# Performance work log

Measured on AMD Instinct MI355X. Metric: run time of the kernel, lower is better.

Reference implementation:

```python
import jax, jax.numpy as jnp
from jax import lax
import numpy as np

ALPHA = 4.0  # spikingjelly surrogate.Sigmoid default alpha
TAU = 2.0
VTH = 1.0

@jax.custom_vjp
def heaviside(x):
    return (x >= 0).astype(x.dtype)

def _h_fwd(x):
    return heaviside(x), x

def _h_bwd(x, g):
    s = jax.nn.sigmoid(ALPHA * x)
    return (g * ALPHA * s * (1.0 - s),)

heaviside.defvjp(_h_fwd, _h_bwd)

def lif(x_seq):
    # MultiStepLIFNode: v += (x - v)/tau, hard reset to 0, detach_reset=True
    def step(v, x):
        v = v + (x - v) / TAU
        s = heaviside(v - VTH)
        v = v * (1.0 - lax.stop_gradient(s))
        return v, s
    _, spikes = lax.scan(step, jnp.zeros_like(x_seq[0]), x_seq)
    return spikes

def ss2d(x, in_w, conv_w, x_proj_w, dt_w, dt_b, A_logs, Ds, ln_g, ln_b, out_w):
    Bn, D, H, W = x.shape
    L = H * W
    x = jnp.einsum('bchw,dc->bdhw', x, in_w)                 # in_proj 1x1, no bias
    x = lax.conv_general_dilated(x, conv_w, (1, 1), 'SAME',
                                 feature_group_count=D)      # depthwise 3x3, no bias
    x = jax.nn.silu(x)
    x0 = x.reshape(Bn, D, L)
    x1 = x.transpose(0, 1, 3, 2).reshape(Bn, D, L)           # W-major scan
    xs = jnp.stack([x0, x1, x0[..., ::-1], x1[..., ::-1]], axis=1)  # (B,4,D,L) cross-scan
    R = dt_w.shape[-1]
    dbl = jnp.einsum('bkdl,krd->bkrl', xs, x_proj_w)         # (B,4,R+2N,L), N=1
    dts, Bs, Cs = dbl[:, :, :R], dbl[:, :, R:R + 1], dbl[:, :, R + 1:R + 2]
    dt = jnp.einsum('bkrl,kdr->bkdl', dts, dt_w)
    dt = jax.nn.softplus(dt + dt_b[None, :, :, None])
    A = -jnp.exp(A_logs)                                     # (4,D), d_state=1
    da = jnp.exp(dt * A[None, :, :, None])
    db = dt * Bs * xs                                        # Bs broadcasts over D
    def comb(l, r):
        al, bl = l
        ar, br = r
        return al * ar, bl * ar + br
    _, h = lax.associative_scan(comb, (da, db), axis=-1)     # h_t = da_t*h_{t-1} + db_t
    ys = Cs * h + Ds[None, :, :, None] * xs                  # (B,4,D,L)
    ya = ys[:, 0] + ys[:, 2, :, ::-1]
    yb = (ys[:, 1] + ys[:, 3, :, ::-1]).reshape(Bn, D, W, H).transpose(0, 1, 3, 2)
    y = ya.reshape(Bn, D, H, W) + yb                         # cross-merge
    mu = y.mean(axis=1, keepdims=True)                       # LayerNorm over channels
    var = jnp.mean((y - mu) ** 2, axis=1, keepdims=True)
    y = (y - mu) * lax.rsqrt(var + 1e-5) * ln_g[None, :, None, None] + ln_b[None, :, None, None]
    return jnp.einsum('bdhw,cd->bchw', y, out_w)             # out_proj 1x1, no bias

def spike_mamba(x, in_proj_w, in_proj_b, conv_w, conv_b, ssm_in_w, ssm_conv_w,
                x_proj_w, dt_proj_w, dt_proj_b, A_logs, Ds, ln_g, ln_b, out_proj_w):
    T, B, C, H, W = x.shape
    TB = T * B
    L = H * W
    xf = x.reshape(TB, C, L).transpose(0, 2, 1)              # (TB, L, C)
    xp = (xf @ in_proj_w.T + in_proj_b).transpose(0, 2, 1).reshape(TB, C, H, W)
    xsnn = lif(xp)                                           # LIF scans over dim 0 (= T*B, as in source)
    xc = lax.conv_general_dilated(xsnn, conv_w, (1, 1), 'SAME') + conv_b[None, :, None, None]
    xc = jax.nn.silu(xc)
    y = ss2d(xc, ssm_in_w, ssm_conv_w, x_proj_w, dt_proj_w, dt_proj_b,
             A_logs, Ds, ln_g, ln_b, out_proj_w)
    y = lif(y.reshape(T, B, C, H, W))                        # LIF over T
    return y * x

def setup_inputs() -> dict:
    key = jax.random.key(0)
    ks = jax.random.split(key, 10)
    T, B, C, H, W = 4, 4, 96, 56, 56
    R, K = 6, 4  # dt_rank=ceil(C/16), 4 scan directions
    s = 1.0 / np.sqrt(C)
    return {
        'x': jax.random.normal(ks[0], (T, B, C, H, W), jnp.float32),
        'in_proj_w': jax.random.normal(ks[1], (C, C), jnp.float32) * s,
        'in_proj_b': jnp.zeros((C,), jnp.float32),
        'conv_w': jax.random.normal(ks[2], (C, C, 3, 3), jnp.float32) * (s / 3.0),
        'conv_b': jnp.zeros((C,), jnp.float32),
        'ssm_in_w': jax.random.normal(ks[3], (C, C), jnp.float32) * s,
        'ssm_conv_w': jax.random.normal(ks[4], (C, 1, 3, 3), jnp.float32) * (1.0 / 3.0),
        'x_proj_w': jax.random.normal(ks[5], (K, R + 2, C), jnp.float32) * s,
        'dt_proj_w': jax.random.normal(ks[6], (K, C, R), jnp.float32) * (1.0 / np.sqrt(R)),
        'dt_proj_b': jax.random.normal(ks[7], (K, C), jnp.float32) * 0.1,
        'A_logs': jax.random.uniform(ks[8], (K, C), jnp.float32, 0.0, 1.0),
        'Ds': jnp.ones((K, C), jnp.float32),
        'ln_g': jnp.ones((C,), jnp.float32),
        'ln_b': jnp.zeros((C,), jnp.float32),
        'out_proj_w': jax.random.normal(ks[9], (C, C), jnp.float32) * s,
    }

def reference(x, in_proj_w, in_proj_b, conv_w, conv_b, ssm_in_w, ssm_conv_w,
              x_proj_w, dt_proj_w, dt_proj_b, A_logs, Ds, ln_g, ln_b, out_proj_w):
    return spike_mamba(x, in_proj_w, in_proj_b, conv_w, conv_b, ssm_in_w, ssm_conv_w,
                       x_proj_w, dt_proj_w, dt_proj_b, A_logs, Ds, ln_g, ln_b, out_proj_w)
```

## Files before the change

### kernel.cpp

```cpp
#include <hip/hip_runtime.h>
#include <math.h>

#define TBn 16
#define Lpx 3136
#define CHW 301056
#define SZn 4816896
#define PRJ 1605632
#define NPAD 3328

__device__ __forceinline__ float siluf_(float z){ return z / (1.f + expf(-z)); }

__global__ __launch_bounds__(256) void k_matmul(const float* __restrict__ in, const float* __restrict__ Wm,
                                                const float* __restrict__ bias, float* __restrict__ out){
  int blk = blockIdx.x;
  int n = blk / 49, pt = blk % 49, p0 = pt * 64;
  __shared__ float lx[96*64];
  __shared__ float wl[96*100];
  int tid = threadIdx.x;
  const float* inb = in + (size_t)n*CHW;
  for (int i = tid; i < 96*64; i += 256){
    int ci = i >> 6, px = i & 63;
    lx[i] = inb[(size_t)ci*Lpx + p0 + px];
  }
  for (int i = tid; i < 96*96; i += 256){
    int co = i / 96, ci = i % 96;
    wl[co*100 + ci] = Wm[i];
  }
  int px_t = tid & 15, co_t = tid >> 4;
  float acc[6][4];
  #pragma unroll
  for (int j = 0; j < 6; ++j){
    float b = bias ? bias[co_t*6 + j] : 0.f;
    #pragma unroll
    for (int q = 0; q < 4; ++q) acc[j][q] = b;
  }
  __syncthreads();
  for (int c4 = 0; c4 < 24; ++c4){
    float4 xv0 = *(const float4*)&lx[(c4*4 + 0)*64 + px_t*4];
    float4 xv1 = *(const float4*)&lx[(c4*4 + 1)*64 + px_t*4];
    float4 xv2 = *(const float4*)&lx[(c4*4 + 2)*64 + px_t*4];
    float4 xv3 = *(const float4*)&lx[(c4*4 + 3)*64 + px_t*4];
    #pragma unroll
    for (int j = 0; j < 6; ++j){
      float4 wv = *(const float4*)&wl[(co_t*6 + j)*100 + c4*4];
      acc[j][0] = fmaf(wv.x, xv0.x, acc[j][0]); acc[j][1] = fmaf(wv.x, xv0.y, acc[j][1]);
      acc[j][2] = fmaf(wv.x, xv0.z, acc[j][2]); acc[j][3] = fmaf(wv.x, xv0.w, acc[j][3]);
      acc[j][0] = fmaf(wv.y, xv1.x, acc[j][0]); acc[j][1] = fmaf(wv.y, xv1.y, acc[j][1]);
      acc[j][2] = fmaf(wv.y, xv1.z, acc[j][2]); acc[j][3] = fmaf(wv.y, xv1.w, acc[j][3]);
      acc[j][0] = fmaf(wv.z, xv2.x, acc[j][0]); acc[j][1] = fmaf(wv.z, xv2.y, acc[j][1]);
      acc[j][2] = fmaf(wv.z, xv2.z, acc[j][2]); acc[j][3] = fmaf(wv.z, xv2.w, acc[j][3]);
      acc[j][0] = fmaf(wv.w, xv3.x, acc[j][0]); acc[j][1] = fmaf(wv.w, xv3.y, acc[j][1]);
      acc[j][2] = fmaf(wv.w, xv3.z, acc[j][2]); acc[j][3] = fmaf(wv.w, xv3.w, acc[j][3]);
    }
  }
  float* ob = out + (size_t)n*CHW + p0 + px_t*4;
  #pragma unroll
  for (int j = 0; j < 6; ++j){
    float4 v; v.x = acc[j][0]; v.y = acc[j][1]; v.z = acc[j][2]; v.w = acc[j][3];
    *(float4*)&ob[(size_t)(co_t*6 + j)*Lpx] = v;
  }
}

__global__ __launch_bounds__(256) void k_matmulM(const float* __restrict__ pA, const float* __restrict__ pB,
                                                 const float* __restrict__ pC, const float* __restrict__ cbias,
                                                 const float* __restrict__ Wm, float* __restrict__ out){
  int blk = blockIdx.x;
  int n = blk / 49, pt = blk % 49, p0 = pt * 64;
  __shared__ float lx[96*64];
  __shared__ float wl[96*100];
  int tid = threadIdx.x;
  const float* inA = pA + (size_t)n*CHW;
  const float* inB = pB + (size_t)n*CHW;
  const float* inC = pC + (size_t)n*CHW;
  for (int i = tid; i < 96*64; i += 256){
    int ci = i >> 6, px = i & 63;
    size_t off = (size_t)ci*Lpx + p0 + px;
    float z = inA[off] + inB[off] + inC[off] + cbias[ci];
    lx[i] = siluf_(z);
  }
  for (int i = tid; i < 96*96; i += 256){
    int co = i / 96, ci = i % 96;
    wl[co*100 + ci] = Wm[i];
  }
  int px_t = tid & 15, co_t = tid >> 4;
  float acc[6][4];
  #pragma unroll
  for (int j = 0; j < 6; ++j)
    #pragma unroll
    for (int q = 0; q < 4; ++q) acc[j][q] = 0.f;
  __syncthreads();
  for (int c4 = 0; c4 < 24; ++c4){
    float4 xv0 = *(const float4*)&lx[(c4*4 + 0)*64 + px_t*4];
    float4 xv1 = *(const float4*)&lx[(c4*4 + 1)*64 + px_t*4];
    float4 xv2 = *(const float4*)&lx[(c4*4 + 2)*64 + px_t*4];
    float4 xv3 = *(const float4*)&lx[(c4*4 + 3)*64 + px_t*4];
    #pragma unroll
    for (int j = 0; j < 6; ++j){
      float4 wv = *(const float4*)&wl[(co_t*6 + j)*100 + c4*4];
      acc[j][0] = fmaf(wv.x, xv0.x, acc[j][0]); acc[j][1] = fmaf(wv.x, xv0.y, acc[j][1]);
      acc[j][2] = fmaf(wv.x, xv0.z, acc[j][2]); acc[j][3] = fmaf(wv.x, xv0.w, acc[j][3]);
      acc[j][0] = fmaf(wv.y, xv1.x, acc[j][0]); acc[j][1] = fmaf(wv.y, xv1.y, acc[j][1]);
      acc[j][2] = fmaf(wv.y, xv1.z, acc[j][2]); acc[j][3] = fmaf(wv.y, xv1.w, acc[j][3]);
      acc[j][0] = fmaf(wv.z, xv2.x, acc[j][0]); acc[j][1] = fmaf(wv.z, xv2.y, acc[j][1]);
      acc[j][2] = fmaf(wv.z, xv2.z, acc[j][2]); acc[j][3] = fmaf(wv.z, xv2.w, acc[j][3]);
      acc[j][0] = fmaf(wv.w, xv3.x, acc[j][0]); acc[j][1] = fmaf(wv.w, xv3.y, acc[j][1]);
      acc[j][2] = fmaf(wv.w, xv3.z, acc[j][2]); acc[j][3] = fmaf(wv.w, xv3.w, acc[j][3]);
    }
  }
  float* ob = out + (size_t)n*CHW + p0 + px_t*4;
  #pragma unroll
  for (int j = 0; j < 6; ++j){
    float4 v; v.x = acc[j][0]; v.y = acc[j][1]; v.z = acc[j][2]; v.w = acc[j][3];
    *(float4*)&ob[(size_t)(co_t*6 + j)*Lpx] = v;
  }
}

__global__ __launch_bounds__(256) void k_lif1(const float* __restrict__ xp, unsigned char* __restrict__ sp){
  int i4 = blockIdx.x*256 + threadIdx.x;
  float4 v = {0.f,0.f,0.f,0.f};
  #pragma unroll
  for (int t = 0; t < 16; ++t){
    float4 z = *(const float4*)&xp[(size_t)t*CHW + (size_t)i4*4];
    v.x = 0.5f*(v.x + z.x); v.y = 0.5f*(v.y + z.y);
    v.z = 0.5f*(v.z + z.z); v.w = 0.5f*(v.w + z.w);
    uchar4 s;
    s.x = (v.x >= 1.0f); s.y = (v.y >= 1.0f); s.z = (v.z >= 1.0f); s.w = (v.w >= 1.0f);
    *(uchar4*)&sp[(size_t)t*CHW + (size_t)i4*4] = s;
    v.x = s.x ? 0.f : v.x; v.y = s.y ? 0.f : v.y;
    v.z = s.z ? 0.f : v.z; v.w = s.w ? 0.f : v.w;
  }
}

#define CIC3 8
__global__ __launch_bounds__(256) void k_conv7(const unsigned char* __restrict__ spk, const float* __restrict__ cw,
                                               float* __restrict__ outP0, float* __restrict__ outP1,
                                               float* __restrict__ outP2){
  int b = blockIdx.x;
  int cog = blockIdx.y % 3, ks = blockIdx.y / 3;
  int hb = blockIdx.z;
  int co0 = cog*32, h0 = hb*8;
  int tid = threadIdx.x;
  int wid = tid >> 6, lane = tid & 63;
  int hl = lane >> 3, wq = lane & 7;
  int coo = __builtin_amdgcn_readfirstlane(wid);
  __shared__ float xl[CIC3*10*68];
  float acc[8][8];
  #pragma unroll
  for (int j = 0; j < 8; ++j)
    #pragma unroll
    for (int q = 0; q < 8; ++q) acc[j][q] = 0.f;

  for (int cc = ks*4; cc < ks*4 + 4; ++cc){
    __syncthreads();
    for (int i = tid; i < CIC3*10*58; i += 256){
      int ci = i / 580, rem = i % 580;
      int hh = rem / 58, ww = rem % 58;
      int sh = h0 - 1 + hh, sw = ww - 1;
      float v = 0.f;
      if (sh >= 0 && sh < 56 && sw >= 0 && sw < 56)
        v = (float)spk[(((size_t)b*96 + cc*CIC3 + ci)*56 + sh)*56 + sw];
      xl[ci*680 + hh*68 + ww] = v;
    }
    __syncthreads();
    for (int ci = 0; ci < CIC3; ++ci){
      int cig = cc*CIC3 + ci;
      float wj[9][8];
      #pragma unroll
      for (int tap = 0; tap < 9; ++tap)
        #pragma unroll
        for (int j = 0; j < 8; ++j)
          wj[tap][j] = cw[(((size_t)(co0 + coo*8 + j))*96 + cig)*9 + tap];
      float xr[3][10];
      int base = ci*680 + hl*68 + wq*8;
      #pragma unroll
      for (int dh = 0; dh < 3; ++dh){
        float4 a = *(const float4*)&xl[base + dh*68];
        float4 c = *(const float4*)&xl[base + dh*68 + 4];
        float2 e = *(const float2*)&xl[base + dh*68 + 8];
        xr[dh][0] = a.x; xr[dh][1] = a.y; xr[dh][2] = a.z; xr[dh][3] = a.w;
        xr[dh][4] = c.x; xr[dh][5] = c.y; xr[dh][6] = c.z; xr[dh][7] = c.w;
        xr[dh][8] = e.x; xr[dh][9] = e.y;
      }
      #pragma unroll
      for (int tap = 0; tap < 9; ++tap){
        const int dh = tap/3, dw = tap%3;
        #pragma unroll
        for (int q = 0; q < 8; ++q){
          float xv = xr[dh][q + dw];
          acc[0][q] = fmaf(xv, wj[tap][0], acc[0][q]);
          acc[1][q] = fmaf(xv, wj[tap][1], acc[1][q]);
          acc[2][q] = fmaf(xv, wj[tap][2], acc[2][q]);
          acc[3][q] = fmaf(xv, wj[tap][3], acc[3][q]);
          acc[4][q] = fmaf(xv, wj[tap][4], acc[4][q]);
          acc[5][q] = fmaf(xv, wj[tap][5], acc[5][q]);
          acc[6][q] = fmaf(xv, wj[tap][6], acc[6][q]);
          acc[7][q] = fmaf(xv, wj[tap][7], acc[7][q]);
        }
      }
    }
  }
  if (wq < 7){
    float* outp = (ks == 0) ? outP0 : (ks == 1) ? outP1 : outP2;
    #pragma unroll
    for (int j = 0; j < 8; ++j){
      int co = co0 + coo*8 + j;
      float4 o0, o1;
      o0.x = acc[j][0]; o0.y = acc[j][1]; o0.z = acc[j][2]; o0.w = acc[j][3];
      o1.x = acc[j][4]; o1.y = acc[j][5]; o1.z = acc[j][6]; o1.w = acc[j][7];
      float* op = &outp[(((size_t)b*96 + co)*56 + h0 + hl)*56 + wq*8];
      *(float4*)op = o0;
      *(float4*)(op + 4) = o1;
    }
  }
}

__global__ __launch_bounds__(256) void k_dwconv(const float* __restrict__ xin, const float* __restrict__ dwW,
                                                float* __restrict__ out, float* __restrict__ outT){
  int bd = blockIdx.x;
  int d = bd % 96;
  const float* ip = xin + (size_t)bd*Lpx;
  __shared__ float pl[Lpx];
  __shared__ float po[Lpx + 56];
  int tid = threadIdx.x;
  for (int i = tid; i < Lpx; i += 256) pl[i] = ip[i];
  float w9[9];
  #pragma unroll
  for (int t = 0; t < 9; ++t) w9[t] = dwW[d*9 + t];
  __syncthreads();
  for (int i = tid; i < Lpx; i += 256){
    int h = i / 56, w = i % 56;
    float s = 0.f;
    #pragma unroll
    for (int tap = 0; tap < 9; ++tap){
      int hh = h + tap/3 - 1, ww = w + tap%3 - 1;
      if (hh >= 0 && hh < 56 && ww >= 0 && ww < 56) s = fmaf(pl[hh*56 + ww], w9[tap], s);
    }
    po[i + i/56] = siluf_(s);
  }
  __syncthreads();
  float* op  = out  + (size_t)bd*Lpx;
  float* otp = outT + (size_t)bd*Lpx;
  for (int i = tid; i < Lpx; i += 256){
    op[i] = po[i + i/56];
    int q = (i % 56)*56 + i/56;
    otp[i] = po[q + q/56];
  }
}

__global__ __launch_bounds__(256) void k_proj(const float* __restrict__ xss, const float* __restrict__ xpw,
                                              float* __restrict__ PROJ, float* __restrict__ PROJT){
  int b = blockIdx.x / 56, h = blockIdx.x % 56;
  __shared__ float lx[96*56];
  __shared__ float lw[32*96];
  int tid = threadIdx.x;
  const float* xb = xss + (size_t)b*CHW + h*56;
  for (int i = tid; i < 96*56; i += 256){
    int d = i / 56, w = i % 56;
    lx[i] = xb[(size_t)d*Lpx + w];
  }
  for (int i = tid; i < 32*96; i += 256) lw[i] = xpw[i];
  __syncthreads();
  for (int o = tid; o < 32*56; o += 256){
    int w = o % 56, kr = o / 56;
    float s = 0.f;
    for (int d = 0; d < 96; ++d) s = fmaf(lx[d*56 + w], lw[kr*96 + d], s);
    size_t base = ((size_t)b*32 + kr)*Lpx;
    PROJ[base + h*56 + w] = s;
    PROJT[base + w*56 + h] = s;
  }
}

__global__ __launch_bounds__(256) void k_scan3(const float* __restrict__ x_rm, const float* __restrict__ x_cm,
                                               const float* __restrict__ PROJ, const float* __restrict__ PROJT,
                                               const float* __restrict__ dtw_all, const float* __restrict__ dtb_all,
                                               const float* __restrict__ Alog, const float* __restrict__ Dall,
                                               float* __restrict__ out0, float* __restrict__ out1){
  int bd = blockIdx.x; int b = bd / 96, d = bd % 96;
  int klo = blockIdx.y;
  const float* xv = (klo == 0 ? x_rm : x_cm) + (size_t)bd*Lpx;
  const float* PR = (klo == 0 ? PROJ : PROJT);
  float* yo = (klo == 0 ? out0 : out1) + (size_t)bd*Lpx;
  int kA = klo, kB = klo + 2;
  const float L2E = 1.44269504f, LN2 = 0.69314718f;

  float dwA[6], dwB[6];
  #pragma unroll
  for (int r = 0; r < 6; ++r){ dwA[r] = dtw_all[(kA*96 + d)*6 + r]; dwB[r] = dtw_all[(kB*96 + d)*6 + r]; }
  float biA = dtb_all[kA*96 + d], biB = dtb_all[kB*96 + d];
  float AA = -expf(Alog[kA*96 + d]) * L2E;
  float AB = -expf(Alog[kB*96 + d]) * L2E;
  float Dsum = Dall[kA*96 + d] + Dall[kB*96 + d];
  const float* pA = PR + ((size_t)b*32 + kA*8)*Lpx;
  const float* pB = PR + ((size_t)b*32 + kB*8)*Lpx;

  __shared__ float u[NPAD];
  __shared__ float v[NPAD];
  __shared__ float yacc[Lpx + 56];
  __shared__ float wag[8];

  int tid = threadIdx.x;
  int lane = tid & 63, wv = tid >> 6;
  int base = tid * 13;
  float la[13], lb[13];

  for (int i = tid; i < Lpx; i += 256){
    float z = biA;
    #pragma unroll
    for (int r = 0; r < 6; ++r) z = fmaf(dwA[r], pA[(size_t)r*Lpx + i], z);
    float t = exp2f(-fabsf(z) * L2E);
    float dt = fmaxf(z, 0.f) + LN2 * log2f(1.f + t);
    u[i] = exp2f(dt * AA);
    v[i] = dt * pA[(size_t)6*Lpx + i] * xv[i];
  }
  for (int i = Lpx + tid; i < NPAD; i += 256){ u[i] = 1.f; v[i] = 0.f; }
  __syncthreads();

  {
    float a = 1.f, bb = 0.f;
    #pragma unroll
    for (int j = 0; j < 13; ++j){
      float da = u[base + j], db = v[base + j];
      bb = fmaf(da, bb, db);
      a *= da;
      la[j] = a; lb[j] = bb;
    }
    float aT = a, bT = bb;
    #pragma unroll
    for (int off = 1; off < 64; off <<= 1){
      float ap = __shfl_up(aT, off), bp = __shfl_up(bT, off);
      if (lane >= off){ bT = fmaf(aT, bp, bT); aT *= ap; }
    }
    if (lane == 63){ wag[wv] = aT; wag[4 + wv] = bT; }
    float a_ex = __shfl_up(aT, 1), b_ex = __shfl_up(bT, 1);
    if (lane == 0){ a_ex = 1.f; b_ex = 0.f; }
    __syncthreads();
    float hw = 0.f;
    for (int j = 0; j < wv; ++j) hw = fmaf(wag[j], hw, wag[4 + j]);
    float hin = fmaf(a_ex, hw, b_ex);
    #pragma unroll
    for (int j = 0; j < 13; ++j)
      v[base + j] = fmaf(la[j], hin, lb[j]);
  }
  __syncthreads();
  for (int i = tid; i < Lpx; i += 256){
    float C = pA[(size_t)7*Lpx + i];
    yacc[i + i/56] = fmaf(C, v[i], Dsum * xv[i]);
  }
  __syncthreads();

  for (int i = tid; i < Lpx; i += 256){
    float z = biB;
    #pragma unroll
    for (int r = 0; r < 6; ++r) z = fmaf(dwB[r], pB[(size_t)r*Lpx + i], z);
    float t = exp2f(-fabsf(z) * L2E);
    float dt = fmaxf(z, 0.f) + LN2 * log2f(1.f + t);
    u[i] = exp2f(dt * AB);
    v[i] = dt * pB[(size_t)6*Lpx + i] * xv[i];
  }
  for (int i = Lpx + tid; i < NPAD; i += 256){ u[i] = 1.f; v[i] = 0.f; }
  __syncthreads();

  {
    float a = 1.f, bb = 0.f;
    #pragma unroll
    for (int j = 12; j >= 0; --j){
      float da = u[base + j], db = v[base + j];
      bb = fmaf(da, bb, db);
      a *= da;
      la[j] = a; lb[j] = bb;
    }
    float aT = a, bT = bb;
    #pragma unroll
    for (int off = 1; off < 64; off <<= 1){
      float ap = __shfl_down(aT, off), bp = __shfl_down(bT, off);
      if (lane + off < 64){ bT = fmaf(aT, bp, bT); aT *= ap; }
    }
    if (lane == 0){ wag[wv] = aT; wag[4 + wv] = bT; }
    float a_ex = __shfl_down(aT, 1), b_ex = __shfl_down(bT, 1);
    if (lane == 63){ a_ex = 1.f; b_ex = 0.f; }
    __syncthreads();
    float hw = 0.f;
    for (int j = 3; j > wv; --j) hw = fmaf(wag[j], hw, wag[4 + j]);
    float hin = fmaf(a_ex, hw, b_ex);
    #pragma unroll
    for (int j = 0; j < 13; ++j)
      v[base + j] = fmaf(la[j], hin, lb[j]);
  }
  __syncthreads();
  for (int i = tid; i < Lpx; i += 256){
    float C = pB[(size_t)7*Lpx + i];
    yacc[i + i/56] = fmaf(C, v[i], yacc[i + i/56]);
  }
  __syncthreads();

  if (klo == 0){
    for (int i = tid; i < Lpx; i += 256)
      yo[i] = yacc[i + i/56];
  } else {
    for (int i = tid; i < Lpx; i += 256){
      int q = (i % 56)*56 + i/56;
      yo[i] = yacc[q + q/56];
    }
  }
}

__global__ __launch_bounds__(256) void k_ln(const float* __restrict__ ya, const float* __restrict__ yb,
                                            const float* __restrict__ g, const float* __restrict__ be,
                                            float* __restrict__ out){
  int i4 = blockIdx.x*256 + threadIdx.x;
  int b = i4 / 784, p = (i4 % 784) * 4;
  const float* ap = ya + (size_t)b*CHW + p;
  const float* bp = yb + (size_t)b*CHW + p;
  float4 s = {0.f,0.f,0.f,0.f};
  for (int d = 0; d < 96; ++d){
    float4 av = *(const float4*)&ap[(size_t)d*Lpx];
    float4 bv = *(const float4*)&bp[(size_t)d*Lpx];
    s.x += av.x + bv.x; s.y += av.y + bv.y; s.z += av.z + bv.z; s.w += av.w + bv.w;
  }
  float4 mu; mu.x = s.x*(1.f/96.f); mu.y = s.y*(1.f/96.f); mu.z = s.z*(1.f/96.f); mu.w = s.w*(1.f/96.f);
  float4 ss = {0.f,0.f,0.f,0.f};
  for (int d = 0; d < 96; ++d){
    float4 av = *(const float4*)&ap[(size_t)d*Lpx];
    float4 bv = *(const float4*)&bp[(size_t)d*Lpx];
    float vx = av.x + bv.x - mu.x, vy = av.y + bv.y - mu.y;
    float vz = av.z + bv.z - mu.z, vw = av.w + bv.w - mu.w;
    ss.x = fmaf(vx,vx,ss.x); ss.y = fmaf(vy,vy,ss.y); ss.z = fmaf(vz,vz,ss.z); ss.w = fmaf(vw,vw,ss.w);
  }
  float4 rs;
  rs.x = 1.f/sqrtf(ss.x*(1.f/96.f) + 1e-5f); rs.y = 1.f/sqrtf(ss.y*(1.f/96.f) + 1e-5f);
  rs.z = 1.f/sqrtf(ss.z*(1.f/96.f) + 1e-5f); rs.w = 1.f/sqrtf(ss.w*(1.f/96.f) + 1e-5f);
  float* op = out + (size_t)b*CHW + p;
  for (int d = 0; d < 96; ++d){
    float4 av = *(const float4*)&ap[(size_t)d*Lpx];
    float4 bv = *(const float4*)&bp[(size_t)d*Lpx];
    float gd = g[d], bd = be[d];
    float4 o;
    o.x = (av.x + bv.x - mu.x)*rs.x*gd + bd;
    o.y = (av.y + bv.y - mu.y)*rs.y*gd + bd;
    o.z = (av.z + bv.z - mu.z)*rs.z*gd + bd;
    o.w = (av.w + bv.w - mu.w)*rs.w*gd + bd;
    *(float4*)&op[(size_t)d*Lpx] = o;
  }
}

__global__ __launch_bounds__(256) void k_lif2(const float* __restrict__ yo, const float* __restrict__ x0,
                                              float* __restrict__ out){
  const int stride4 = 301056;
  int i4 = blockIdx.x*256 + threadIdx.x;
  float4 v = {0.f,0.f,0.f,0.f};
  #pragma unroll
  for (int t = 0; t < 4; ++t){
    float4 z = *(const float4*)&yo[((size_t)t*stride4 + i4)*4];
    float4 xv = *(const float4*)&x0[((size_t)t*stride4 + i4)*4];
    v.x = 0.5f*(v.x + z.x); v.y = 0.5f*(v.y + z.y);
    v.z = 0.5f*(v.z + z.z); v.w = 0.5f*(v.w + z.w);
    float4 o;
    o.x = (v.x >= 1.0f) ? xv.x : 0.f; o.y = (v.y >= 1.0f) ? xv.y : 0.f;
    o.z = (v.z >= 1.0f) ? xv.z : 0.f; o.w = (v.w >= 1.0f) ? xv.w : 0.f;
    v.x = (v.x >= 1.0f) ? 0.f : v.x; v.y = (v.y >= 1.0f) ? 0.f : v.y;
    v.z = (v.z >= 1.0f) ? 0.f : v.z; v.w = (v.w >= 1.0f) ? 0.f : v.w;
    *(float4*)&out[((size_t)t*stride4 + i4)*4] = o;
  }
}

extern "C" void kernel_launch(void* const* d_in, const int* in_sizes, int n_in,
                              void* d_out, int out_size, void* d_ws, size_t ws_size,
                              hipStream_t stream) {
  const float* x    = (const float*)d_in[0];
  const float* ipw  = (const float*)d_in[1];
  const float* ipb  = (const float*)d_in[2];
  const float* cw   = (const float*)d_in[3];
  const float* cb   = (const float*)d_in[4];
  const float* siw  = (const float*)d_in[5];
  const float* scw  = (const float*)d_in[6];
  const float* xpw  = (const float*)d_in[7];
  const float* dtw  = (const float*)d_in[8];
  const float* dtb  = (const float*)d_in[9];
  const float* alog = (const float*)d_in[10];
  const float* dsv  = (const float*)d_in[11];
  const float* lng  = (const float*)d_in[12];
  const float* lnb  = (const float*)d_in[13];
  const float* opw  = (const float*)d_in[14];

  float* s1 = (float*)d_ws;
  float* s2 = s1 + SZn;
  float* s3 = s2 + SZn;
  float* s4 = s3 + SZn;
  float* pr  = s4 + SZn;
  float* prT = pr + PRJ;

  k_matmul<<<784, 256, 0, stream>>>(x, ipw, ipb, s1);
  k_lif1<<<294, 256, 0, stream>>>(s1, (unsigned char*)s2);
  k_conv7<<<dim3(16, 9, 7), 256, 0, stream>>>((const unsigned char*)s2, cw, s1, s3, s4);
  k_matmulM<<<784, 256, 0, stream>>>(s1, s3, s4, cb, siw, s2);
  k_dwconv<<<1536, 256, 0, stream>>>(s2, scw, s1, s3);
  k_proj<<<896, 256, 0, stream>>>(s1, xpw, pr, prT);
  k_scan3<<<dim3(1536, 2), 256, 0, stream>>>(s1, s3, pr, prT, dtw, dtb, alog, dsv, s2, s4);
  k_ln<<<49, 256, 0, stream>>>(s2, s4, lng, lnb, s3);
  k_matmul<<<784, 256, 0, stream>>>(s3, opw, nullptr, s2);
  k_lif2<<<1176, 256, 0, stream>>>(s2, x, (float*)d_out);
}
```

Baseline: 475.9 us.

## Fuse LayerNorm into out-projection matmul and prefetch conv tiles via registers

The separate LayerNorm kernel is removed. Its work (summing the two scan outputs, per-pixel channel mean and variance, scale and shift) now runs inside the out-projection matmul on the shared-memory tile. This drops one full-tensor write and read and a kernel launch that used only 49 blocks. The 3x3 conv kernel now loads the next channel chunk into registers while it computes the current one, overlapping global loads with FMAs. The cost is higher register pressure, which may reduce occupancy.

Result: faster. 434.9 us (-8.6%).

```diff
diff --git a/kernel.cpp b/kernel.cpp
--- a/kernel.cpp
+++ b/kernel.cpp
@@ -115,6 +115,83 @@
   }
 }
 
+__global__ __launch_bounds__(256) void k_matmulLN(const float* __restrict__ ya, const float* __restrict__ yb,
+                                                  const float* __restrict__ g, const float* __restrict__ be,
+                                                  const float* __restrict__ Wm, float* __restrict__ out){
+  int blk = blockIdx.x;
+  int n = blk / 49, pt = blk % 49, p0 = pt * 64;
+  __shared__ float lx[96*64];
+  __shared__ float wl[96*100];
+  __shared__ float red[4*64];
+  __shared__ float muS[64], rsS[64];
+  int tid = threadIdx.x;
+  const float* inA = ya + (size_t)n*CHW;
+  const float* inB = yb + (size_t)n*CHW;
+  for (int i = tid; i < 96*64; i += 256){
+    int ci = i >> 6, px = i & 63;
+    size_t off = (size_t)ci*Lpx + p0 + px;
+    lx[i] = inA[off] + inB[off];
+  }
+  for (int i = tid; i < 96*96; i += 256){
+    int co = i / 96, ci = i % 96;
+    wl[co*100 + ci] = Wm[i];
+  }
+  __syncthreads();
+  int pxr = tid & 63, gq = tid >> 6;
+  {
+    float s = 0.f;
+    for (int c = 0; c < 24; ++c) s += lx[(gq*24 + c)*64 + pxr];
+    red[gq*64 + pxr] = s;
+  }
+  __syncthreads();
+  if (tid < 64) muS[tid] = (red[tid] + red[64+tid] + red[128+tid] + red[192+tid]) * (1.f/96.f);
+  __syncthreads();
+  {
+    float m = muS[pxr];
+    float q = 0.f;
+    for (int c = 0; c < 24; ++c){ float v = lx[(gq*24 + c)*64 + pxr] - m; q = fmaf(v, v, q); }
+    red[gq*64 + pxr] = q;
+  }
+  __syncthreads();
+  if (tid < 64) rsS[tid] = 1.f / sqrtf((red[tid] + red[64+tid] + red[128+tid] + red[192+tid])*(1.f/96.f) + 1e-5f);
+  __syncthreads();
+  for (int i = tid; i < 96*64; i += 256){
+    int ci = i >> 6, ppx = i & 63;
+    lx[i] = (lx[i] - muS[ppx]) * rsS[ppx] * g[ci] + be[ci];
+  }
+  int px_t = tid & 15, co_t = tid >> 4;
+  float acc[6][4];
+  #pragma unroll
+  for (int j = 0; j < 6; ++j)
+    #pragma unroll
+    for (int q = 0; q < 4; ++q) acc[j][q] = 0.f;
+  __syncthreads();
+  for (int c4 = 0; c4 < 24; ++c4){
+    float4 xv0 = *(const float4*)&lx[(c4*4 + 0)*64 + px_t*4];
+    float4 xv1 = *(const float4*)&lx[(c4*4 + 1)*64 + px_t*4];
+    float4 xv2 = *(const float4*)&lx[(c4*4 + 2)*64 + px_t*4];
+    float4 xv3 = *(const float4*)&lx[(c4*4 + 3)*64 + px_t*4];
+    #pragma unroll
+    for (int j = 0; j < 6; ++j){
+      float4 wv = *(const float4*)&wl[(co_t*6 + j)*100 + c4*4];
+      acc[j][0] = fmaf(wv.x, xv0.x, acc[j][0]); acc[j][1] = fmaf(wv.x, xv0.y, acc[j][1]);
+      acc[j][2] = fmaf(wv.x, xv0.z, acc[j][2]); acc[j][3] = fmaf(wv.x, xv0.w, acc[j][3]);
+      acc[j][0] = fmaf(wv.y, xv1.x, acc[j][0]); acc[j][1] = fmaf(wv.y, xv1.y, acc[j][1]);
+      acc[j][2] = fmaf(wv.y, xv1.z, acc[j][2]); acc[j][3] = fmaf(wv.y, xv1.w, acc[j][3]);
+      acc[j][0] = fmaf(wv.z, xv2.x, acc[j][0]); acc[j][1] = fmaf(wv.z, xv2.y, acc[j][1]);
+      acc[j][2] = fmaf(wv.z, xv2.z, acc[j][2]); acc[j][3] = fmaf(wv.z, xv2.w, acc[j][3]);
+      acc[j][0] = fmaf(wv.w, xv3.x, acc[j][0]); acc[j][1] = fmaf(wv.w, xv3.y, acc[j][1]);
+      acc[j][2] = fmaf(wv.w, xv3.z, acc[j][2]); acc[j][3] = fmaf(wv.w, xv3.w, acc[j][3]);
+    }
+  }
+  float* ob = out + (size_t)n*CHW + p0 + px_t*4;
+  #pragma unroll
+  for (int j = 0; j < 6; ++j){
+    float4 v; v.x = acc[j][0]; v.y = acc[j][1]; v.z = acc[j][2]; v.w = acc[j][3];
+    *(float4*)&ob[(size_t)(co_t*6 + j)*Lpx] = v;
+  }
+}
+
 __global__ __launch_bounds__(256) void k_lif1(const float* __restrict__ xp, unsigned char* __restrict__ sp){
   int i4 = blockIdx.x*256 + threadIdx.x;
   float4 v = {0.f,0.f,0.f,0.f};
@@ -132,7 +209,8 @@
 }
 
 #define CIC3 8
-__global__ __launch_bounds__(256) void k_conv7(const unsigned char* __restrict__ spk, const float* __restrict__ cw,
+#define NST 19
+__global__ __launch_bounds__(256) void k_conv8(const unsigned char* __restrict__ spk, const float* __restrict__ cw,
                                                float* __restrict__ outP0, float* __restrict__ outP1,
                                                float* __restrict__ outP2){
   int b = blockIdx.x;
@@ -144,24 +222,50 @@
   int hl = lane >> 3, wq = lane & 7;
   int coo = __builtin_amdgcn_readfirstlane(wid);
   __shared__ float xl[CIC3*10*68];
+  const unsigned char* spb = spk + (size_t)b*96*3136;
   float acc[8][8];
   #pragma unroll
   for (int j = 0; j < 8; ++j)
     #pragma unroll
     for (int q = 0; q < 8; ++q) acc[j][q] = 0.f;
 
-  for (int cc = ks*4; cc < ks*4 + 4; ++cc){
-    __syncthreads();
-    for (int i = tid; i < CIC3*10*58; i += 256){
-      int ci = i / 580, rem = i % 580;
-      int hh = rem / 58, ww = rem % 58;
-      int sh = h0 - 1 + hh, sw = ww - 1;
-      float v = 0.f;
-      if (sh >= 0 && sh < 56 && sw >= 0 && sw < 56)
-        v = (float)spk[(((size_t)b*96 + cc*CIC3 + ci)*56 + sh)*56 + sw];
-      xl[ci*680 + hh*68 + ww] = v;
-    }
-    __syncthreads();
+  {
+    int cc = ks*4;
+    #pragma unroll
+    for (int j = 0; j < NST; ++j){
+      int i = tid + j*256;
+      if (i < CIC3*10*58){
+        int ci = i / 580, rem = i % 580;
+        int hh = rem / 58, ww = rem % 58;
+        int sh = h0 - 1 + hh, sw = ww - 1;
+        float v = 0.f;
+        if (sh >= 0 && sh < 56 && sw >= 0 && sw < 56)
+          v = (float)spb[(size_t)(cc*CIC3 + ci)*3136 + sh*56 + sw];
+        xl[ci*680 + hh*68 + ww] = v;
+      }
+    }
+  }
+  __syncthreads();
+
+  for (int s = 0; s < 4; ++s){
+    int cc = ks*4 + s;
+    float f2[NST];
+    if (s < 3){
+      int cn = cc + 1;
+      #pragma unroll
+      for (int j = 0; j < NST; ++j){
+        int i = tid + j*256;
+        float v = 0.f;
+        if (i < CIC3*10*58){
+          int ci = i / 580, rem = i % 580;
+          int hh = rem / 58, ww = rem % 58;
+          int sh = h0 - 1 + hh, sw = ww - 1;
+          if (sh >= 0 && sh < 56 && sw >= 0 && sw < 56)
+            v = (float)spb[(size_t)(cn*CIC3 + ci)*3136 + sh*56 + sw];
+        }
+        f2[j] = v;
+      }
+    }
     for (int ci = 0; ci < CIC3; ++ci){
       int cig = cc*CIC3 + ci;
       float wj[9][8];
@@ -198,6 +302,19 @@
         }
       }
     }
+    __syncthreads();
+    if (s < 3){
+      #pragma unroll
+      for (int j = 0; j < NST; ++j){
+        int i = tid + j*256;
+        if (i < CIC3*10*58){
+          int ci = i / 580, rem = i % 580;
+          int hh = rem / 58, ww = rem % 58;
+          xl[ci*680 + hh*68 + ww] = f2[j];
+        }
+      }
+      __syncthreads();
+    }
   }
   if (wq < 7){
     float* outp = (ks == 0) ? outP0 : (ks == 1) ? outP1 : outP2;
@@ -401,45 +518,6 @@
       int q = (i % 56)*56 + i/56;
       yo[i] = yacc[q + q/56];
     }
-  }
-}
-
-__global__ __launch_bounds__(256) void k_ln(const float* __restrict__ ya, const float* __restrict__ yb,
-                                            const float* __restrict__ g, const float* __restrict__ be,
-                                            float* __restrict__ out){
-  int i4 = blockIdx.x*256 + threadIdx.x;
-  int b = i4 / 784, p = (i4 % 784) * 4;
-  const float* ap = ya + (size_t)b*CHW + p;
-  const float* bp = yb + (size_t)b*CHW + p;
-  float4 s = {0.f,0.f,0.f,0.f};
-  for (int d = 0; d < 96; ++d){
-    float4 av = *(const float4*)&ap[(size_t)d*Lpx];
-    float4 bv = *(const float4*)&bp[(size_t)d*Lpx];
-    s.x += av.x + bv.x; s.y += av.y + bv.y; s.z += av.z + bv.z; s.w += av.w + bv.w;
-  }
-  float4 mu; mu.x = s.x*(1.f/96.f); mu.y = s.y*(1.f/96.f); mu.z = s.z*(1.f/96.f); mu.w = s.w*(1.f/96.f);
-  float4 ss = {0.f,0.f,0.f,0.f};
-  for (int d = 0; d < 96; ++d){
-    float4 av = *(const float4*)&ap[(size_t)d*Lpx];
-    float4 bv = *(const float4*)&bp[(size_t)d*Lpx];
-    float vx = av.x + bv.x - mu.x, vy = av.y + bv.y - mu.y;
-    float vz = av.z + bv.z - mu.z, vw = av.w + bv.w - mu.w;
-    ss.x = fmaf(vx,vx,ss.x); ss.y = fmaf(vy,vy,ss.y); ss.z = fmaf(vz,vz,ss.z); ss.w = fmaf(vw,vw,ss.w);
-  }
-  float4 rs;
-  rs.x = 1.f/sqrtf(ss.x*(1.f/96.f) + 1e-5f); rs.y = 1.f/sqrtf(ss.y*(1.f/96.f) + 1e-5f);
-  rs.z = 1.f/sqrtf(ss.z*(1.f/96.f) + 1e-5f); rs.w = 1.f/sqrtf(ss.w*(1.f/96.f) + 1e-5f);
-  float* op = out + (size_t)b*CHW + p;
-  for (int d = 0; d < 96; ++d){
-    float4 av = *(const float4*)&ap[(size_t)d*Lpx];
-    float4 bv = *(const float4*)&bp[(size_t)d*Lpx];
-    float gd = g[d], bd = be[d];
-    float4 o;
-    o.x = (av.x + bv.x - mu.x)*rs.x*gd + bd;
-    o.y = (av.y + bv.y - mu.y)*rs.y*gd + bd;
-    o.z = (av.z + bv.z - mu.z)*rs.z*gd + bd;
-    o.w = (av.w + bv.w - mu.w)*rs.w*gd + bd;
-    *(float4*)&op[(size_t)d*Lpx] = o;
   }
 }
 
@@ -491,12 +569,11 @@
 
   k_matmul<<<784, 256, 0, stream>>>(x, ipw, ipb, s1);
   k_lif1<<<294, 256, 0, stream>>>(s1, (unsigned char*)s2);
-  k_conv7<<<dim3(16, 9, 7), 256, 0, stream>>>((const unsigned char*)s2, cw, s1, s3, s4);
+  k_conv8<<<dim3(16, 9, 7), 256, 0, stream>>>((const unsigned char*)s2, cw, s1, s3, s4);
   k_matmulM<<<784, 256, 0, stream>>>(s1, s3, s4, cb, siw, s2);
   k_dwconv<<<1536, 256, 0, stream>>>(s2, scw, s1, s3);
   k_proj<<<896, 256, 0, stream>>>(s1, xpw, pr, prT);
   k_scan3<<<dim3(1536, 2), 256, 0, stream>>>(s1, s3, pr, prT, dtw, dtb, alog, dsv, s2, s4);
-  k_ln<<<49, 256, 0, stream>>>(s2, s4, lng, lnb, s3);
-  k_matmul<<<784, 256, 0, stream>>>(s3, opw, nullptr, s2);
-  k_lif2<<<1176, 256, 0, stream>>>(s2, x, (float*)d_out);
-}
+  k_matmulLN<<<784, 256, 0, stream>>>(s2, s4, lng, lnb, opw, s1);
+  k_lif2<<<1176, 256, 0, stream>>>(s1, x, (float*)d_out);
+}
```
